# Kernel tuning notes

Measured on AMD Instinct MI355X. Metric: run time of the kernel, lower is better.

Reference implementation:

```python
import jax, jax.numpy as jnp
import numpy as np

C, H, W, NC, LC = 512, 160, 160, 1203, 64


def setup_inputs() -> dict:
    key = jax.random.key(0)
    ks = jax.random.split(key, 8)
    return {
        "cls_feat": jax.random.normal(ks[0], (1, C, H, W), jnp.float32),
        "loc_feat": jax.random.normal(ks[1], (1, LC, H, W), jnp.float32),
        "conf": jax.random.uniform(ks[2], (1,), jnp.float32, 0.2, 0.8),
        "pf_w": jax.random.normal(ks[3], (C,), jnp.float32) * 0.02,   # pf 1x1 conv, C->1
        "pf_b": jnp.zeros((1,), jnp.float32),
        "vocab_w": jax.random.normal(ks[4], (NC, C), jnp.float32) * 0.02,  # conv2linear weight
        "vocab_b": jnp.zeros((NC,), jnp.float32),
        "loc_w": jax.random.normal(ks[5], (LC, LC), jnp.float32) * 0.02,   # loc 1x1 conv
        "loc_b": jnp.zeros((LC,), jnp.float32),
    }


def reference(cls_feat, loc_feat, conf, pf_w, pf_b, vocab_w, vocab_b, loc_w, loc_b):
    B, Cc, Hh, Ww = cls_feat.shape
    # proposal-filter score: 1x1 conv C->1 on batch 0, flattened to [HW]
    pf_score = jnp.einsum('c,chw->hw', pf_w, cls_feat[0]).reshape(-1) + pf_b  # [HW]
    mask = jax.nn.sigmoid(pf_score) > conf[0]  # [HW] bool
    # tokens: [1, HW, C]
    tok = cls_feat.reshape(B, Cc, Hh * Ww).transpose(0, 2, 1)
    # static-shape equivalent of the proposal filter: zero masked-out tokens
    tok = tok * mask[None, :, None].astype(tok.dtype)
    # vocab linear (converted 1x1 conv): [1, HW, NC] -> [1, NC, HW]
    cls_out = (jnp.einsum('bnc,vc->bnv', tok, vocab_w) + vocab_b).transpose(0, 2, 1)
    # localization 1x1 conv
    loc_out = jnp.einsum('oi,bihw->bohw', loc_w, loc_feat) + loc_b[None, :, None, None]
    return loc_out, cls_out, mask
```

## Files before the change

### kernel.cpp

```cpp
#include <hip/hip_runtime.h>
#include <math.h>


constexpr int C_    = 512;
constexpr int HW_   = 25600;
constexpr int NC_   = 1203;
constexpr int VPAD_ = 1216;

constexpr int LOC_OFF_  = 0;
constexpr int CLS_OFF_  = 64 * HW_;
constexpr int MASK_OFF_ = CLS_OFF_ + NC_ * HW_;

constexpr int PF_BLOCKS_    = HW_ / 64;
constexpr int TRANS_BLOCKS_ = 19 * 8;
constexpr int LOC_BLOCKS_   = 400;
constexpr int FILL_BLOCKS_  = 2048;

typedef float vfloat4 __attribute__((ext_vector_type(4)));

__global__ void k_init(int* cnt) { *cnt = 0; }

__global__ __launch_bounds__(256) void k_pre(
    const float* __restrict__ cls_feat, const float* __restrict__ conf,
    const float* __restrict__ pf_w, const float* __restrict__ pf_b,
    const float* __restrict__ vocab_w, float* __restrict__ out,
    int* __restrict__ cnt, int* __restrict__ idxList,
    int* __restrict__ jLut, float* __restrict__ AT4, int jcap)
{
    const int bid = blockIdx.x;
    const int tid = threadIdx.x;

    if (bid < PF_BLOCKS_) {
        __shared__ double sPart[256];
        const int hwi   = tid & 63;
        const int slice = tid >> 6;
        const int hw    = bid * 64 + hwi;
        const float* p  = cls_feat + (size_t)slice * 128 * HW_ + hw;
        const float* w  = pf_w + slice * 128;
        double acc = 0.0;
        #pragma unroll 4
        for (int k = 0; k < 128; ++k)
            acc += (double)w[k] * (double)p[(size_t)k * HW_];
        sPart[tid] = acc;
        __syncthreads();
        if (slice == 0) {
            double s = sPart[hwi] + sPart[64 + hwi] + sPart[128 + hwi] +
                       sPart[192 + hwi] + (double)pf_b[0];
            double sig = 1.0 / (1.0 + exp(-s));
            bool m = sig > (double)conf[0];
            out[MASK_OFF_ + hw] = m ? 1.0f : 0.0f;
            int pos = -1;
            if (m) {
                pos = atomicAdd(cnt, 1);
                if (pos < HW_) idxList[pos] = hw;
            }
            jLut[hw] = (m && pos >= 0 && pos < jcap) ? pos : -1;
        }
    } else {
        if (jcap <= 0) return;
        const int tb = bid - PF_BLOCKS_;
        const int v0 = (tb % 19) * 64;
        const int k0 = (tb / 19) * 64;
        __shared__ float t[64][65];
        const int c  = tid & 63;
        const int r4 = tid >> 6;
        #pragma unroll
        for (int i = 0; i < 16; ++i) {
            const int r = r4 * 16 + i;
            const int v = v0 + r;
            t[r][c] = (v < NC_) ? vocab_w[(size_t)v * C_ + k0 + c] : 0.f;
        }
        __syncthreads();
        #pragma unroll
        for (int i = 0; i < 16; ++i) {
            const int k  = r4 * 16 + i;
            const int kg = k0 + k;
            AT4[((size_t)(kg >> 2) * VPAD_ + v0 + c) * 4 + (kg & 3)] = t[c][k];
        }
    }
}

__global__ __launch_bounds__(256) void k_gatherJ(
    const float* __restrict__ cls_feat, const int* __restrict__ cnt,
    const int* __restrict__ idxList, float* __restrict__ BdT, int jcap)
{
    const int count = min(*cnt, HW_);
    if (count > jcap) return;
    const int t = threadIdx.x;
    for (int j = blockIdx.x; j < count; j += gridDim.x) {
        const int hw = idxList[j];
        BdT[(size_t)j * C_ + t]       = cls_feat[(size_t)t * HW_ + hw];
        BdT[(size_t)j * C_ + 256 + t] = cls_feat[(size_t)(256 + t) * HW_ + hw];
    }
}

__global__ __launch_bounds__(256) void k_gemm6t(
    const float* __restrict__ AT4, const float* __restrict__ vocab_b,
    const int* __restrict__ cnt, const float* __restrict__ BdT,
    float* __restrict__ clsTmp, int jcap)
{
    const int count = min(*cnt, HW_);
    if (count == 0 || count > jcap) return;
    const int jBase = blockIdx.y * 4;
    if (jBase >= count) return;

    const int tid  = threadIdx.x;
    const int lane = tid & 63;
    const int w    = __builtin_amdgcn_readfirstlane(tid >> 6);
    const int v0   = blockIdx.x * 64;
    const int v    = v0 + lane;
    const float* __restrict__ Acol = AT4 + (size_t)v * 4;

    const int j0 = jBase + 0, j1 = jBase + 1, j2 = jBase + 2, j3 = jBase + 3;
    const float* __restrict__ B0 = BdT + (size_t)(j0 < count ? j0 : 0) * C_;
    const float* __restrict__ B1 = BdT + (size_t)(j1 < count ? j1 : 0) * C_;
    const float* __restrict__ B2 = BdT + (size_t)(j2 < count ? j2 : 0) * C_;
    const float* __restrict__ B3 = BdT + (size_t)(j3 < count ? j3 : 0) * C_;

    vfloat4 ac0 = {0,0,0,0}, ac1 = {0,0,0,0}, ac2 = {0,0,0,0}, ac3 = {0,0,0,0};
    const int kqBeg = w * 32;
    #pragma unroll 8
    for (int q = 0; q < 32; ++q) {
        const int kq = kqBeg + q;
        const vfloat4 a  = *(const vfloat4*)(Acol + (size_t)kq * VPAD_ * 4);
        const vfloat4 b0 = *(const vfloat4*)(B0 + kq * 4);
        const vfloat4 b1 = *(const vfloat4*)(B1 + kq * 4);
        const vfloat4 b2 = *(const vfloat4*)(B2 + kq * 4);
        const vfloat4 b3 = *(const vfloat4*)(B3 + kq * 4);
        ac0 += a * b0; ac1 += a * b1; ac2 += a * b2; ac3 += a * b3;
    }

    __shared__ float sRed[4][4][64];
    sRed[w][0][lane] = (ac0.x + ac0.y) + (ac0.z + ac0.w);
    sRed[w][1][lane] = (ac1.x + ac1.y) + (ac1.z + ac1.w);
    sRed[w][2][lane] = (ac2.x + ac2.y) + (ac2.z + ac2.w);
    sRed[w][3][lane] = (ac3.x + ac3.y) + (ac3.z + ac3.w);
    __syncthreads();

    if (tid < 64) {
        const float bias = (v < NC_) ? vocab_b[v] : 0.f;
        #pragma unroll
        for (int jj = 0; jj < 4; ++jj) {
            const int j = jBase + jj;
            if (j < count) {
                const float s =
                    (sRed[0][jj][lane] + sRed[1][jj][lane]) +
                    (sRed[2][jj][lane] + sRed[3][jj][lane]);
                clsTmp[(size_t)j * VPAD_ + v] = s + bias;
            }
        }
    }
}

__global__ __launch_bounds__(256) void k_mega(
    const float* __restrict__ loc_feat, const float* __restrict__ vocab_b,
    const float* __restrict__ loc_w, const float* __restrict__ loc_b,
    const int* __restrict__ cnt, const int* __restrict__ jLut,
    const float* __restrict__ clsTmp, float* __restrict__ out, int jcap)
{
    const int bid = blockIdx.x;
    const int tid = threadIdx.x;

    if (bid < LOC_BLOCKS_) {
        const int j   = bid;
        const int hwb = j % 100;
        const int o0  = (j / 100) * 16;
        __shared__ float sw[16][64];
        for (int i = tid; i < 16 * 64; i += 256)
            sw[i >> 6][i & 63] = loc_w[(o0 + (i >> 6)) * 64 + (i & 63)];
        __syncthreads();
        const int hw = hwb * 256 + tid;
        float acc[16];
        #pragma unroll
        for (int r = 0; r < 16; ++r) acc[r] = loc_b[o0 + r];
        for (int i = 0; i < 64; ++i) {
            float f = loc_feat[(size_t)i * HW_ + hw];
            #pragma unroll
            for (int r = 0; r < 16; ++r) acc[r] += sw[r][i] * f;
        }
        #pragma unroll
        for (int r = 0; r < 16; ++r)
            out[LOC_OFF_ + (size_t)(o0 + r) * HW_ + hw] = acc[r];
    } else {
        const int fb     = bid - LOC_BLOCKS_;
        const int count  = min(*cnt, HW_);
        const bool live  = (jcap > 0) && (count > 0) && (count <= jcap);
        const int hw4    = HW_ / 4;
        const int total4 = NC_ * HW_ / 4;
        const int4* jLut4 = (const int4*)jLut;
        vfloat4* o = (vfloat4*)(out + CLS_OFF_);
        for (int i = fb * 256 + tid; i < total4; i += FILL_BLOCKS_ * 256) {
            const int v   = i / hw4;
            const int rem = i - v * hw4;
            const float b = vocab_b[v];
            vfloat4 val = {b, b, b, b};
            if (live) {
                const int4 jl = jLut4[rem];
                if ((jl.x | jl.y | jl.z | jl.w) >= 0 ||
                    jl.x >= 0 || jl.y >= 0 || jl.z >= 0 || jl.w >= 0) {
                    if (jl.x >= 0) val.x = clsTmp[(size_t)jl.x * VPAD_ + v];
                    if (jl.y >= 0) val.y = clsTmp[(size_t)jl.y * VPAD_ + v];
                    if (jl.z >= 0) val.z = clsTmp[(size_t)jl.z * VPAD_ + v];
                    if (jl.w >= 0) val.w = clsTmp[(size_t)jl.w * VPAD_ + v];
                }
            }
            __builtin_nontemporal_store(val, &o[i]);
        }
    }
}

__global__ __launch_bounds__(256) void k_gemm_fallback(
    const float* __restrict__ cls_feat, const float* __restrict__ vocab_w,
    const float* __restrict__ vocab_b, const int* __restrict__ cnt,
    const int* __restrict__ idxList, float* __restrict__ out, int capB)
{
    const int count = min(*cnt, HW_);
    if (count <= capB) return;
    const int v0 = blockIdx.x * 64;

    __shared__ float sAT[16][64];
    __shared__ float sBT[16][64];
    __shared__ int   sIdx[64];

    const int tid = threadIdx.x;
    const int tx = tid & 15;
    const int ty = tid >> 4;
    const int r  = tid >> 2;
    const int kq = tid & 3;

    for (int jb = blockIdx.y; (jb << 6) < count; jb += gridDim.y) {
        const int j0 = jb << 6;
        __syncthreads();
        if (tid < 64) {
            int j = j0 + tid;
            sIdx[tid] = (j < count) ? idxList[j] : -1;
        }
        __syncthreads();
        const int hwj = sIdx[r];

        float acc[4][4] = {};
        for (int k0 = 0; k0 < C_; k0 += 16) {
            float4 a4 = make_float4(0.f, 0.f, 0.f, 0.f);
            if (v0 + r < NC_)
                a4 = *(const float4*)(vocab_w + (size_t)(v0 + r) * C_ + k0 + kq * 4);
            float b0 = 0.f, b1 = 0.f, b2 = 0.f, b3 = 0.f;
            if (hwj >= 0) {
                const float* bp = cls_feat + (size_t)(k0 + kq * 4) * HW_ + hwj;
                b0 = bp[0]; b1 = bp[HW_]; b2 = bp[2 * HW_]; b3 = bp[3 * HW_];
            }
            __syncthreads();
            sAT[kq * 4 + 0][r] = a4.x; sAT[kq * 4 + 1][r] = a4.y;
            sAT[kq * 4 + 2][r] = a4.z; sAT[kq * 4 + 3][r] = a4.w;
            sBT[kq * 4 + 0][r] = b0;   sBT[kq * 4 + 1][r] = b1;
            sBT[kq * 4 + 2][r] = b2;   sBT[kq * 4 + 3][r] = b3;
            __syncthreads();
            #pragma unroll
            for (int kk = 0; kk < 16; ++kk) {
                const float4 av = *(const float4*)&sAT[kk][ty * 4];
                const float4 bv = *(const float4*)&sBT[kk][tx * 4];
                acc[0][0] += av.x * bv.x; acc[0][1] += av.x * bv.y;
                acc[0][2] += av.x * bv.z; acc[0][3] += av.x * bv.w;
                acc[1][0] += av.y * bv.x; acc[1][1] += av.y * bv.y;
                acc[1][2] += av.y * bv.z; acc[1][3] += av.y * bv.w;
                acc[2][0] += av.z * bv.x; acc[2][1] += av.z * bv.y;
                acc[2][2] += av.z * bv.z; acc[2][3] += av.z * bv.w;
                acc[3][0] += av.w * bv.x; acc[3][1] += av.w * bv.y;
                acc[3][2] += av.w * bv.z; acc[3][3] += av.w * bv.w;
            }
        }
        #pragma unroll
        for (int a = 0; a < 4; ++a) {
            int v = v0 + ty * 4 + a;
            if (v >= NC_) continue;
            float bias = vocab_b[v];
            #pragma unroll
            for (int b = 0; b < 4; ++b) {
                int j = j0 + tx * 4 + b;
                if (j < count) {
                    int hw = sIdx[tx * 4 + b];
                    out[CLS_OFF_ + (size_t)v * HW_ + hw] = acc[a][b] + bias;
                }
            }
        }
    }
}

extern "C" void kernel_launch(void* const* d_in, const int* in_sizes, int n_in,
                              void* d_out, int out_size, void* d_ws,
                              size_t ws_size, hipStream_t stream) {
    const float* cls_feat = (const float*)d_in[0];
    const float* loc_feat = (const float*)d_in[1];
    const float* conf     = (const float*)d_in[2];
    const float* pf_w     = (const float*)d_in[3];
    const float* pf_b     = (const float*)d_in[4];
    const float* vocab_w  = (const float*)d_in[5];
    const float* vocab_b  = (const float*)d_in[6];
    const float* loc_w    = (const float*)d_in[7];
    const float* loc_b    = (const float*)d_in[8];
    float* out = (float*)d_out;

    int*   cnt      = (int*)d_ws;
    int*   idxList  = (int*)((char*)d_ws + 4096);
    int*   jLut     = (int*)((char*)d_ws + 4096 + (size_t)HW_ * 4);
    size_t fixed    = 4096 + (size_t)HW_ * 4 * 2;
    size_t atBytes  = (size_t)(C_ / 4) * VPAD_ * 4 * sizeof(float);
    size_t bdtBytes = (size_t)1024 * C_ * sizeof(float);
    size_t tmpBytes = (size_t)1024 * VPAD_ * sizeof(float);
    float* AT4      = (float*)((char*)d_ws + fixed);
    float* BdT      = (float*)((char*)d_ws + fixed + atBytes);
    float* clsTmp   = (float*)((char*)d_ws + fixed + atBytes + bdtBytes);

    int jcap = 0;
    if (ws_size >= fixed + atBytes + bdtBytes + tmpBytes) jcap = 1024;

    hipLaunchKernelGGL(k_init, dim3(1), dim3(1), 0, stream, cnt);
    hipLaunchKernelGGL(k_pre, dim3(PF_BLOCKS_ + TRANS_BLOCKS_), dim3(256),
                       0, stream,
                       cls_feat, conf, pf_w, pf_b, vocab_w, out, cnt,
                       idxList, jLut, AT4, jcap);
    if (jcap > 0) {
        hipLaunchKernelGGL(k_gatherJ, dim3(512), dim3(256), 0, stream,
                           cls_feat, cnt, idxList, BdT, jcap);
        hipLaunchKernelGGL(k_gemm6t, dim3(19, 1024 / 4), dim3(256), 0, stream,
                           AT4, vocab_b, cnt, BdT, clsTmp, jcap);
    }
    hipLaunchKernelGGL(k_mega, dim3(LOC_BLOCKS_ + FILL_BLOCKS_), dim3(256),
                       0, stream,
                       loc_feat, vocab_b, loc_w, loc_b, cnt, jLut, clsTmp,
                       out, jcap);
    hipLaunchKernelGGL(k_gemm_fallback, dim3((NC_ + 63) / 64, 8), dim3(256),
                       0, stream, cls_feat, vocab_w, vocab_b, cnt, idxList,
                       out, jcap);
}
```

Before: 70.23 us.

## Keep vocab weight slice in registers and stream selected tokens through LDS

The sparse vocab GEMM now gives each block a fixed 64-class slice of the transposed weights, loaded once into registers (32 float4 per thread). Selected token columns are then streamed through shared memory, with the next token prefetched while the current one is computed. The grid shrinks from 19x256 to 19x8 blocks. This stops the weight slice being re-read from global memory for every group of four tokens, at the cost of high register pressure, three barriers per token and far fewer blocks to hide latency. A redundant condition in the fill kernel is also simplified.

```diff
diff --git a/kernel.cpp b/kernel.cpp
--- a/kernel.cpp
+++ b/kernel.cpp
@@ -17,6 +17,7 @@
 constexpr int FILL_BLOCKS_  = 2048;
 
 typedef float vfloat4 __attribute__((ext_vector_type(4)));
+typedef float vfloat2 __attribute__((ext_vector_type(2)));
 
 __global__ void k_init(int* cnt) { *cnt = 0; }
 
@@ -94,61 +95,61 @@
     }
 }
 
-__global__ __launch_bounds__(256) void k_gemm6t(
+__global__ __launch_bounds__(256) void k_gemmR(
     const float* __restrict__ AT4, const float* __restrict__ vocab_b,
     const int* __restrict__ cnt, const float* __restrict__ BdT,
     float* __restrict__ clsTmp, int jcap)
 {
     const int count = min(*cnt, HW_);
     if (count == 0 || count > jcap) return;
-    const int jBase = blockIdx.y * 4;
-    if (jBase >= count) return;
 
     const int tid  = threadIdx.x;
     const int lane = tid & 63;
-    const int w    = __builtin_amdgcn_readfirstlane(tid >> 6);
+    const int w    = tid >> 6;
     const int v0   = blockIdx.x * 64;
     const int v    = v0 + lane;
-    const float* __restrict__ Acol = AT4 + (size_t)v * 4;
-
-    const int j0 = jBase + 0, j1 = jBase + 1, j2 = jBase + 2, j3 = jBase + 3;
-    const float* __restrict__ B0 = BdT + (size_t)(j0 < count ? j0 : 0) * C_;
-    const float* __restrict__ B1 = BdT + (size_t)(j1 < count ? j1 : 0) * C_;
-    const float* __restrict__ B2 = BdT + (size_t)(j2 < count ? j2 : 0) * C_;
-    const float* __restrict__ B3 = BdT + (size_t)(j3 < count ? j3 : 0) * C_;
-
-    vfloat4 ac0 = {0,0,0,0}, ac1 = {0,0,0,0}, ac2 = {0,0,0,0}, ac3 = {0,0,0,0};
-    const int kqBeg = w * 32;
-    #pragma unroll 8
+
+    vfloat4 Ar[32];
+    #pragma unroll
     for (int q = 0; q < 32; ++q) {
-        const int kq = kqBeg + q;
-        const vfloat4 a  = *(const vfloat4*)(Acol + (size_t)kq * VPAD_ * 4);
-        const vfloat4 b0 = *(const vfloat4*)(B0 + kq * 4);
-        const vfloat4 b1 = *(const vfloat4*)(B1 + kq * 4);
-        const vfloat4 b2 = *(const vfloat4*)(B2 + kq * 4);
-        const vfloat4 b3 = *(const vfloat4*)(B3 + kq * 4);
-        ac0 += a * b0; ac1 += a * b1; ac2 += a * b2; ac3 += a * b3;
-    }
-
-    __shared__ float sRed[4][4][64];
-    sRed[w][0][lane] = (ac0.x + ac0.y) + (ac0.z + ac0.w);
-    sRed[w][1][lane] = (ac1.x + ac1.y) + (ac1.z + ac1.w);
-    sRed[w][2][lane] = (ac2.x + ac2.y) + (ac2.z + ac2.w);
-    sRed[w][3][lane] = (ac3.x + ac3.y) + (ac3.z + ac3.w);
-    __syncthreads();
-
-    if (tid < 64) {
-        const float bias = (v < NC_) ? vocab_b[v] : 0.f;
-        #pragma unroll
-        for (int jj = 0; jj < 4; ++jj) {
-            const int j = jBase + jj;
-            if (j < count) {
-                const float s =
-                    (sRed[0][jj][lane] + sRed[1][jj][lane]) +
-                    (sRed[2][jj][lane] + sRed[3][jj][lane]);
-                clsTmp[(size_t)j * VPAD_ + v] = s + bias;
-            }
-        }
+        const int kq = w * 32 + q;
+        Ar[q] = *(const vfloat4*)(AT4 + ((size_t)kq * VPAD_ + v) * 4);
+    }
+
+    const float bias = (v < NC_) ? vocab_b[v] : 0.f;
+
+    __shared__ float Bs[512];
+    __shared__ float sRed[4][64];
+
+    int j = blockIdx.y;
+    vfloat2 bcur = {0.f, 0.f};
+    if (j < count)
+        bcur = *(const vfloat2*)(BdT + (size_t)j * C_ + tid * 2);
+
+    for (; j < count; j += 8) {
+        *(vfloat2*)&Bs[tid * 2] = bcur;
+        __syncthreads();
+
+        const int jn = j + 8;
+        if (jn < count)
+            bcur = *(const vfloat2*)(BdT + (size_t)jn * C_ + tid * 2);
+
+        vfloat4 acc = {0.f, 0.f, 0.f, 0.f};
+        #pragma unroll
+        for (int q = 0; q < 32; ++q) {
+            const vfloat4 b = *(const vfloat4*)&Bs[(w * 32 + q) * 4];
+            acc += Ar[q] * b;
+        }
+
+        sRed[w][lane] = (acc.x + acc.y) + (acc.z + acc.w);
+        __syncthreads();
+
+        if (tid < 64) {
+            const float s = (sRed[0][lane] + sRed[1][lane]) +
+                            (sRed[2][lane] + sRed[3][lane]);
+            clsTmp[(size_t)j * VPAD_ + v] = s + bias;
+        }
+        __syncthreads();
     }
 }
 
@@ -196,8 +197,7 @@
             vfloat4 val = {b, b, b, b};
             if (live) {
                 const int4 jl = jLut4[rem];
-                if ((jl.x | jl.y | jl.z | jl.w) >= 0 ||
-                    jl.x >= 0 || jl.y >= 0 || jl.z >= 0 || jl.w >= 0) {
+                if (jl.x >= 0 || jl.y >= 0 || jl.z >= 0 || jl.w >= 0) {
                     if (jl.x >= 0) val.x = clsTmp[(size_t)jl.x * VPAD_ + v];
                     if (jl.y >= 0) val.y = clsTmp[(size_t)jl.y * VPAD_ + v];
                     if (jl.z >= 0) val.z = clsTmp[(size_t)jl.z * VPAD_ + v];
@@ -321,7 +321,7 @@
     if (jcap > 0) {
         hipLaunchKernelGGL(k_gatherJ, dim3(512), dim3(256), 0, stream,
                            cls_feat, cnt, idxList, BdT, jcap);
-        hipLaunchKernelGGL(k_gemm6t, dim3(19, 1024 / 4), dim3(256), 0, stream,
+        hipLaunchKernelGGL(k_gemmR, dim3(19, 8), dim3(256), 0, stream,
                            AT4, vocab_b, cnt, BdT, clsTmp, jcap);
     }
     hipLaunchKernelGGL(k_mega, dim3(LOC_BLOCKS_ + FILL_BLOCKS_), dim3(256),
```

Result: slower. 81.85 us (+16.5%).
